# Kernel optimization log

Hardware: AMD Instinct MI355X
Metric: run time of the kernel (lower is better)

Reference implementation:

```python
import jax, jax.numpy as jnp
import numpy as np

BUCKET_SIZE = 64
LOOK_BACKWARD = 1
LOOK_FORWARD = 0  # causal => no look forward
CAUSAL = True


def look_around(x, backward, forward, pad_value):
    # x: [b, buckets, bucket_size, ...]; pads along the bucket axis and concats
    # shifted windows along the intra-bucket axis (dim=2), matching torch look_around.
    t = x.shape[1]
    pad_cfg = ((0, 0), (backward, forward)) + ((0, 0),) * (x.ndim - 2)
    padded = jnp.pad(x, pad_cfg, constant_values=pad_value)
    return jnp.concatenate([padded[:, i:i + t] for i in range(forward + backward + 1)], axis=2)


def setup_inputs() -> dict:
    key = jax.random.key(0)
    kq, kk, kv = jax.random.split(key, 3)
    shape = (4, 16, 4096, 64)  # [batch, heads, seq, head_dim]
    q = jax.random.normal(kq, shape, dtype=jnp.float32)
    k = jax.random.normal(kk, shape, dtype=jnp.float32)
    v = jax.random.normal(kv, shape, dtype=jnp.float32)
    return {"q": q, "k": k, "v": v}


def reference(q, k, v):
    shape = q.shape
    # merge batch and heads
    merge = lambda t: t.reshape(-1, t.shape[-2], t.shape[-1])
    q, k, v = merge(q), merge(k), merge(v)
    b, t, e = q.shape
    assert t % BUCKET_SIZE == 0
    buckets = t // BUCKET_SIZE

    ticker = jnp.arange(t, dtype=jnp.int32)[None, :]          # [1, t]
    b_t = ticker.reshape(1, buckets, BUCKET_SIZE)              # [1, buckets, bucket]

    bucket_fn = lambda x: x.reshape(b, buckets, BUCKET_SIZE, e)
    bq, bk, bv = bucket_fn(q), bucket_fn(k), bucket_fn(v)

    bk = look_around(bk, LOOK_BACKWARD, LOOK_FORWARD, 0.0)
    bv = look_around(bv, LOOK_BACKWARD, LOOK_FORWARD, 0.0)
    bq_t = b_t                                                 # query positions
    bq_k = look_around(b_t, LOOK_BACKWARD, LOOK_FORWARD, -1)   # key positions, -1 = pad

    scale = e ** (-0.5)
    dots = jnp.einsum('bnie,bnje->bnij', bq, bk) * scale
    mask_value = -jnp.finfo(dots.dtype).max

    if CAUSAL:
        causal_mask = bq_t[:, :, :, None] < bq_k[:, :, None, :]
        dots = jnp.where(causal_mask, mask_value, dots)

    pad_mask = bq_k[:, :, None, :] == -1
    dots = jnp.where(pad_mask, mask_value, dots)

    attn = jax.nn.softmax(dots, axis=-1)
    out = jnp.einsum('bnij,bnje->bnie', attn, bv)
    return out.reshape(shape)
```

## Files before the change

kernel.cpp:

```cpp
#include <hip/hip_runtime.h>
#include <hip/hip_bf16.h>

typedef __attribute__((ext_vector_type(8))) __bf16 bf16x8;
typedef __attribute__((ext_vector_type(4))) float f32x4;

#define SEQ   4096
#define HDIM  64
#define BKT   64

__device__ __forceinline__ unsigned f2bf_u(float f) {
    unsigned u = __float_as_uint(f);
    u += 0x7FFFu + ((u >> 16) & 1u);
    return u >> 16;
}
__device__ __forceinline__ unsigned pk2(float a, float b) {
    return f2bf_u(a) | (f2bf_u(b) << 16);
}
__device__ __forceinline__ int swzV(int row) {
    return ((row & 7) ^ ((row >> 3) & 7)) << 4;
}

__global__ void __launch_bounds__(256, 4) local_attn_kernel(
    const float* __restrict__ q, const float* __restrict__ k,
    const float* __restrict__ v, float* __restrict__ out)
{
    __shared__ __align__(16) unsigned short sK[128 * 64];
    __shared__ __align__(16) unsigned short sVt[64 * 128];

    const int tid = threadIdx.x;
    const int bid0 = blockIdx.x;
    const int lg = (bid0 & 7) * 512 + (bid0 >> 3);
    const int bh = lg >> 6;
    const int bucket = lg & 63;

    const int qoff = (bh * SEQ + bucket * BKT) * HDIM;
    const int koff = qoff - BKT * HDIM;
    const int fix0 = (bucket == 0) ? (BKT * HDIM) : 0;

    const int lane = tid & 63;
    const int wid  = tid >> 6;
    const int g = lane >> 4, m = lane & 15;
    const int g4 = g * 4;
    const int qbase = wid * 16;

    char* const sKb = reinterpret_cast<char*>(sK);
    char* const sVb = reinterpret_cast<char*>(sVt);

    f32x4 kreg[8], vreg[8], qreg[4];
    #pragma unroll
    for (int i = 0; i < 8; ++i) {
        const float* p = k + koff + ((i < 4) ? fix0 : 0) + i * 1024 + tid * 4;
        asm volatile("global_load_dwordx4 %0, %1, off"
                     : "=v"(kreg[i]) : "v"(p) : "memory");
    }
    #pragma unroll
    for (int i = 0; i < 8; ++i) {
        const int kb = i * 16 + wid * 4;
        const float* p = v + koff + ((i < 4) ? fix0 : 0) + (kb + g) * HDIM + m * 4;
        asm volatile("global_load_dwordx4 %0, %1, off"
                     : "=v"(vreg[i]) : "v"(p) : "memory");
    }
    #pragma unroll
    for (int h = 0; h < 2; ++h) {
        const float* qp = q + qoff + (qbase + m) * HDIM + h * 32 + g * 8;
        asm volatile("global_load_dwordx4 %0, %1, off"
                     : "=v"(qreg[2 * h]) : "v"(qp) : "memory");
        asm volatile("global_load_dwordx4 %0, %1, off"
                     : "=v"(qreg[2 * h + 1]) : "v"(qp + 4) : "memory");
    }

    asm volatile("s_waitcnt vmcnt(12)" ::: "memory");
    __builtin_amdgcn_sched_barrier(0);
    #pragma unroll
    for (int i = 0; i < 8; ++i) {
        const int flat = i * 1024 + tid * 4;
        const int row = flat >> 6, col = flat & 63;
        uint2 p;
        p.x = pk2(kreg[i][0], kreg[i][1]);
        p.y = pk2(kreg[i][2], kreg[i][3]);
        const int byte = (row * 128 + col * 2) ^ ((row & 7) << 4);
        *reinterpret_cast<uint2*>(sKb + byte) = p;
    }

    asm volatile("s_waitcnt vmcnt(4)" ::: "memory");
    __builtin_amdgcn_sched_barrier(0);
    #pragma unroll
    for (int i = 0; i < 8; ++i) {
        const int kb = i * 16 + wid * 4;
        const f32x4 f = vreg[i];
        const unsigned P0 = pk2(f[0], f[1]);
        const unsigned P1 = pk2(f[2], f[3]);
        const unsigned own  = (g < 2) ? P0 : P1;
        const unsigned send = (g < 2) ? P1 : P0;
        const unsigned R = __shfl_xor(send, 32);
        const unsigned T = __shfl_xor(own, 16);
        const unsigned U = __shfl_xor(R, 16);
        const unsigned A0 = (g < 2) ? own : R;
        const unsigned A1 = (g < 2) ? T : U;
        const unsigned A2 = (g < 2) ? R : own;
        const unsigned A3 = (g < 2) ? U : T;
        const int sdx = g & 1;
        const unsigned k0 = sdx ? A1 : A0, k1 = sdx ? A0 : A1;
        const unsigned k2 = sdx ? A3 : A2, k3 = sdx ? A2 : A3;
        const unsigned G0 = sdx ? ((k0 >> 16) | (k1 & 0xFFFF0000u)) : ((k0 & 0xFFFFu) | (k1 << 16));
        const unsigned G1 = sdx ? ((k2 >> 16) | (k3 & 0xFFFF0000u)) : ((k2 & 0xFFFFu) | (k3 << 16));
        const int er = m * 4 + g;
        const int byte = (er * 256 + kb * 2) ^ swzV(er);
        uint2 p; p.x = G0; p.y = G1;
        *reinterpret_cast<uint2*>(sVb + byte) = p;
    }

    asm volatile("s_waitcnt vmcnt(0)" ::: "memory");
    __builtin_amdgcn_sched_barrier(0);
    const float scale = 0.125f * 1.44269504f;
    bf16x8 bq[2];
    #pragma unroll
    for (int h = 0; h < 2; ++h) {
        uint4 u;
        u.x = pk2(qreg[2 * h][0] * scale, qreg[2 * h][1] * scale);
        u.y = pk2(qreg[2 * h][2] * scale, qreg[2 * h][3] * scale);
        u.z = pk2(qreg[2 * h + 1][0] * scale, qreg[2 * h + 1][1] * scale);
        u.w = pk2(qreg[2 * h + 1][2] * scale, qreg[2 * h + 1][3] * scale);
        bq[h] = __builtin_bit_cast(bf16x8, u);
    }
    __syncthreads();

    f32x4 acc[8];
    #pragma unroll
    for (int c = 0; c < 8; ++c) acc[c] = (f32x4){0.f, 0.f, 0.f, 0.f};
    __builtin_amdgcn_s_setprio(1);
    #pragma unroll
    for (int c = 0; c < 8; ++c) {
        const int krow = c * 16 + m;
        #pragma unroll
        for (int h = 0; h < 2; ++h) {
            const int byte = (krow * 128 + h * 64 + g * 16) ^ ((m & 7) << 4);
            const bf16x8 ak = *reinterpret_cast<const bf16x8*>(sKb + byte);
            acc[c] = __builtin_amdgcn_mfma_f32_16x16x32_bf16(ak, bq[h], acc[c], 0, 0, 0);
        }
    }
    __builtin_amdgcn_s_setprio(0);

    const int qb = qbase + m;
    float mx = -3e38f;
    #pragma unroll
    for (int c = 0; c < 8; ++c) {
        #pragma unroll
        for (int r = 0; r < 4; ++r) {
            const int kk = c * 16 + g4 + r;
            const bool dead = (c >= 4) ? (kk - 64 > qb) : (bucket == 0);
            const float s = dead ? -1e30f : acc[c][r];
            acc[c][r] = s;
            mx = fmaxf(mx, s);
        }
    }
    mx = fmaxf(mx, __shfl_xor(mx, 16));
    mx = fmaxf(mx, __shfl_xor(mx, 32));
    float sum = 0.f;
    uint2 pb[8];
    #pragma unroll
    for (int c = 0; c < 8; ++c) {
        const float p0 = __builtin_amdgcn_exp2f(acc[c][0] - mx);
        const float p1 = __builtin_amdgcn_exp2f(acc[c][1] - mx);
        const float p2 = __builtin_amdgcn_exp2f(acc[c][2] - mx);
        const float p3 = __builtin_amdgcn_exp2f(acc[c][3] - mx);
        sum += (p0 + p1) + (p2 + p3);
        pb[c].x = pk2(p0, p1);
        pb[c].y = pk2(p2, p3);
    }
    sum += __shfl_xor(sum, 16);
    sum += __shfl_xor(sum, 32);
    const float rl = 1.0f / sum;

    const int l0 = m + ((g & 1) << 5);
    const int l1 = l0 + 16;
    const bool hi2 = (g >> 1) != 0;
    bf16x8 bp[4];
    #pragma unroll
    for (int kt = 0; kt < 4; ++kt) {
        const unsigned a0x = __shfl(pb[2 * kt].x, l0),     a0y = __shfl(pb[2 * kt].y, l0);
        const unsigned a1x = __shfl(pb[2 * kt + 1].x, l0), a1y = __shfl(pb[2 * kt + 1].y, l0);
        const unsigned b0x = __shfl(pb[2 * kt].x, l1),     b0y = __shfl(pb[2 * kt].y, l1);
        const unsigned b1x = __shfl(pb[2 * kt + 1].x, l1), b1y = __shfl(pb[2 * kt + 1].y, l1);
        uint4 u;
        u.x = hi2 ? a1x : a0x;
        u.y = hi2 ? a1y : a0y;
        u.z = hi2 ? b1x : b0x;
        u.w = hi2 ? b1y : b0y;
        bp[kt] = __builtin_bit_cast(bf16x8, u);
    }

    f32x4 oacc[4];
    #pragma unroll
    for (int et = 0; et < 4; ++et) oacc[et] = (f32x4){0.f, 0.f, 0.f, 0.f};
    __builtin_amdgcn_s_setprio(1);
    #pragma unroll
    for (int et = 0; et < 4; ++et) {
        const int row = et * 16 + m;
        #pragma unroll
        for (int kt = 0; kt < 4; ++kt) {
            const int byte = (row * 256 + kt * 64 + g * 16) ^ swzV(row);
            const bf16x8 av = *reinterpret_cast<const bf16x8*>(sVb + byte);
            oacc[et] = __builtin_amdgcn_mfma_f32_16x16x32_bf16(av, bp[kt], oacc[et], 0, 0, 0);
        }
    }
    __builtin_amdgcn_s_setprio(0);

    const int qrow = qbase + m;
    #pragma unroll
    for (int et = 0; et < 4; ++et) {
        f32x4 o = oacc[et];
        o[0] *= rl; o[1] *= rl; o[2] *= rl; o[3] *= rl;
        *reinterpret_cast<float4*>(out + qoff + qrow * HDIM + et * 16 + g4) =
            *reinterpret_cast<float4*>(&o);
    }
}

extern "C" void kernel_launch(void* const* d_in, const int* in_sizes, int n_in,
                              void* d_out, int out_size, void* d_ws, size_t ws_size,
                              hipStream_t stream) {
    const float* q = (const float*)d_in[0];
    const float* k = (const float*)d_in[1];
    const float* v = (const float*)d_in[2];
    float* out = (float*)d_out;
    const int bh = in_sizes[0] / (SEQ * HDIM);
    const int nblocks = bh * (SEQ / BKT);
    hipLaunchKernelGGL(local_attn_kernel, dim3(nblocks), dim3(256), 0, stream,
                       q, k, v, out);
}
```

Measured before the change: 46.04 us.

## Process strips of four buckets per block with double-buffered K/V reuse

```diff
diff --git a/kernel.cpp b/kernel.cpp
--- a/kernel.cpp
+++ b/kernel.cpp
@@ -7,6 +7,8 @@
 #define SEQ   4096
 #define HDIM  64
 #define BKT   64
+#define STRIP 4
+#define SLOTB 8192
 
 __device__ __forceinline__ unsigned f2bf_u(float f) {
     unsigned u = __float_as_uint(f);
@@ -20,199 +22,263 @@
     return ((row & 7) ^ ((row >> 3) & 7)) << 4;
 }
 
+__device__ __forceinline__ void vtrans_write(char* sVb, int slotbyte, int kl,
+                                             f32x4 f, int g, int m) {
+    const unsigned P0 = pk2(f[0], f[1]);
+    const unsigned P1 = pk2(f[2], f[3]);
+    const unsigned own  = (g < 2) ? P0 : P1;
+    const unsigned send = (g < 2) ? P1 : P0;
+    const unsigned R = __shfl_xor(send, 32);
+    const unsigned T = __shfl_xor(own, 16);
+    const unsigned U = __shfl_xor(R, 16);
+    const unsigned A0 = (g < 2) ? own : R;
+    const unsigned A1 = (g < 2) ? T : U;
+    const unsigned A2 = (g < 2) ? R : own;
+    const unsigned A3 = (g < 2) ? U : T;
+    const int sdx = g & 1;
+    const unsigned k0 = sdx ? A1 : A0, k1 = sdx ? A0 : A1;
+    const unsigned k2 = sdx ? A3 : A2, k3 = sdx ? A2 : A3;
+    const unsigned G0 = sdx ? ((k0 >> 16) | (k1 & 0xFFFF0000u)) : ((k0 & 0xFFFFu) | (k1 << 16));
+    const unsigned G1 = sdx ? ((k2 >> 16) | (k3 & 0xFFFF0000u)) : ((k2 & 0xFFFFu) | (k3 << 16));
+    const int er = m * 4 + g;
+    const int byte = slotbyte + ((er * 128 + kl * 2) ^ swzV(er));
+    uint2 p; p.x = G0; p.y = G1;
+    *reinterpret_cast<uint2*>(sVb + byte) = p;
+}
+
 __global__ void __launch_bounds__(256, 4) local_attn_kernel(
     const float* __restrict__ q, const float* __restrict__ k,
     const float* __restrict__ v, float* __restrict__ out)
 {
-    __shared__ __align__(16) unsigned short sK[128 * 64];
-    __shared__ __align__(16) unsigned short sVt[64 * 128];
+    __shared__ __align__(16) unsigned short sK[2 * 64 * 64];
+    __shared__ __align__(16) unsigned short sVt[2 * 64 * 64];
 
     const int tid = threadIdx.x;
-    const int bid0 = blockIdx.x;
-    const int lg = (bid0 & 7) * 512 + (bid0 >> 3);
-    const int bh = lg >> 6;
-    const int bucket = lg & 63;
-
-    const int qoff = (bh * SEQ + bucket * BKT) * HDIM;
-    const int koff = qoff - BKT * HDIM;
-    const int fix0 = (bucket == 0) ? (BKT * HDIM) : 0;
+    const int bid = blockIdx.x;
+    const int lg = (bid & 7) * 128 + (bid >> 3);
+    const int bh = lg >> 4;
+    const int strip = lg & 15;
+    const int b0 = strip * STRIP;
+    const int base = bh * SEQ * HDIM;
 
     const int lane = tid & 63;
     const int wid  = tid >> 6;
     const int g = lane >> 4, m = lane & 15;
     const int g4 = g * 4;
     const int qbase = wid * 16;
+    const int qb = qbase + m;
 
     char* const sKb = reinterpret_cast<char*>(sK);
     char* const sVb = reinterpret_cast<char*>(sVt);
 
-    f32x4 kreg[8], vreg[8], qreg[4];
-    #pragma unroll
-    for (int i = 0; i < 8; ++i) {
-        const float* p = k + koff + ((i < 4) ? fix0 : 0) + i * 1024 + tid * 4;
-        asm volatile("global_load_dwordx4 %0, %1, off"
-                     : "=v"(kreg[i]) : "v"(p) : "memory");
-    }
-    #pragma unroll
-    for (int i = 0; i < 8; ++i) {
-        const int kb = i * 16 + wid * 4;
-        const float* p = v + koff + ((i < 4) ? fix0 : 0) + (kb + g) * HDIM + m * 4;
-        asm volatile("global_load_dwordx4 %0, %1, off"
-                     : "=v"(vreg[i]) : "v"(p) : "memory");
-    }
-    #pragma unroll
-    for (int h = 0; h < 2; ++h) {
-        const float* qp = q + qoff + (qbase + m) * HDIM + h * 32 + g * 8;
-        asm volatile("global_load_dwordx4 %0, %1, off"
-                     : "=v"(qreg[2 * h]) : "v"(qp) : "memory");
-        asm volatile("global_load_dwordx4 %0, %1, off"
-                     : "=v"(qreg[2 * h + 1]) : "v"(qp + 4) : "memory");
-    }
-
-    asm volatile("s_waitcnt vmcnt(12)" ::: "memory");
-    __builtin_amdgcn_sched_barrier(0);
-    #pragma unroll
-    for (int i = 0; i < 8; ++i) {
-        const int flat = i * 1024 + tid * 4;
-        const int row = flat >> 6, col = flat & 63;
-        uint2 p;
-        p.x = pk2(kreg[i][0], kreg[i][1]);
-        p.y = pk2(kreg[i][2], kreg[i][3]);
-        const int byte = (row * 128 + col * 2) ^ ((row & 7) << 4);
-        *reinterpret_cast<uint2*>(sKb + byte) = p;
-    }
-
-    asm volatile("s_waitcnt vmcnt(4)" ::: "memory");
-    __builtin_amdgcn_sched_barrier(0);
-    #pragma unroll
-    for (int i = 0; i < 8; ++i) {
-        const int kb = i * 16 + wid * 4;
-        const f32x4 f = vreg[i];
-        const unsigned P0 = pk2(f[0], f[1]);
-        const unsigned P1 = pk2(f[2], f[3]);
-        const unsigned own  = (g < 2) ? P0 : P1;
-        const unsigned send = (g < 2) ? P1 : P0;
-        const unsigned R = __shfl_xor(send, 32);
-        const unsigned T = __shfl_xor(own, 16);
-        const unsigned U = __shfl_xor(R, 16);
-        const unsigned A0 = (g < 2) ? own : R;
-        const unsigned A1 = (g < 2) ? T : U;
-        const unsigned A2 = (g < 2) ? R : own;
-        const unsigned A3 = (g < 2) ? U : T;
-        const int sdx = g & 1;
-        const unsigned k0 = sdx ? A1 : A0, k1 = sdx ? A0 : A1;
-        const unsigned k2 = sdx ? A3 : A2, k3 = sdx ? A2 : A3;
-        const unsigned G0 = sdx ? ((k0 >> 16) | (k1 & 0xFFFF0000u)) : ((k0 & 0xFFFFu) | (k1 << 16));
-        const unsigned G1 = sdx ? ((k2 >> 16) | (k3 & 0xFFFF0000u)) : ((k2 & 0xFFFFu) | (k3 << 16));
-        const int er = m * 4 + g;
-        const int byte = (er * 256 + kb * 2) ^ swzV(er);
-        uint2 p; p.x = G0; p.y = G1;
-        *reinterpret_cast<uint2*>(sVb + byte) = p;
-    }
-
-    asm volatile("s_waitcnt vmcnt(0)" ::: "memory");
-    __builtin_amdgcn_sched_barrier(0);
     const float scale = 0.125f * 1.44269504f;
     bf16x8 bq[2];
+
+    {
+        const int fix0 = (strip == 0) ? (BKT * HDIM) : 0;
+        const int win0 = base + (b0 - 1) * BKT * HDIM;
+        f32x4 kreg[8], vreg[8], qreg[4];
+        #pragma unroll
+        for (int i = 0; i < 8; ++i) {
+            const float* p = k + win0 + ((i < 4) ? fix0 : 0) + i * 1024 + tid * 4;
+            asm volatile("global_load_dwordx4 %0, %1, off" : "=v"(kreg[i]) : "v"(p) : "memory");
+        }
+        #pragma unroll
+        for (int i = 0; i < 8; ++i) {
+            const int kb = i * 16 + wid * 4;
+            const float* p = v + win0 + ((i < 4) ? fix0 : 0) + (kb + g) * HDIM + m * 4;
+            asm volatile("global_load_dwordx4 %0, %1, off" : "=v"(vreg[i]) : "v"(p) : "memory");
+        }
+        const int qoff0 = base + b0 * BKT * HDIM;
+        #pragma unroll
+        for (int h = 0; h < 2; ++h) {
+            const float* qp = q + qoff0 + qb * HDIM + h * 32 + g * 8;
+            asm volatile("global_load_dwordx4 %0, %1, off" : "=v"(qreg[2 * h]) : "v"(qp) : "memory");
+            asm volatile("global_load_dwordx4 %0, %1, off" : "=v"(qreg[2 * h + 1]) : "v"(qp + 4) : "memory");
+        }
+        asm volatile("s_waitcnt vmcnt(12)" ::: "memory");
+        __builtin_amdgcn_sched_barrier(0);
+        #pragma unroll
+        for (int i = 0; i < 8; ++i) {
+            const int flat = i * 1024 + tid * 4;
+            const int lr = (flat >> 6) & 63, col = flat & 63;
+            uint2 p;
+            p.x = pk2(kreg[i][0], kreg[i][1]);
+            p.y = pk2(kreg[i][2], kreg[i][3]);
+            const int byte = ((i < 4) ? SLOTB : 0) + ((lr * 128 + col * 2) ^ ((lr & 7) << 4));
+            *reinterpret_cast<uint2*>(sKb + byte) = p;
+        }
+        asm volatile("s_waitcnt vmcnt(4)" ::: "memory");
+        __builtin_amdgcn_sched_barrier(0);
+        #pragma unroll
+        for (int i = 0; i < 8; ++i) {
+            const int kl = (i * 16 + wid * 4) & 63;
+            vtrans_write(sVb, (i < 4) ? SLOTB : 0, kl, vreg[i], g, m);
+        }
+        asm volatile("s_waitcnt vmcnt(0)" ::: "memory");
+        __builtin_amdgcn_sched_barrier(0);
+        #pragma unroll
+        for (int h = 0; h < 2; ++h) {
+            uint4 u;
+            u.x = pk2(qreg[2 * h][0] * scale, qreg[2 * h][1] * scale);
+            u.y = pk2(qreg[2 * h][2] * scale, qreg[2 * h][3] * scale);
+            u.z = pk2(qreg[2 * h + 1][0] * scale, qreg[2 * h + 1][1] * scale);
+            u.w = pk2(qreg[2 * h + 1][2] * scale, qreg[2 * h + 1][3] * scale);
+            bq[h] = __builtin_bit_cast(bf16x8, u);
+        }
+        __syncthreads();
+    }
+
     #pragma unroll
-    for (int h = 0; h < 2; ++h) {
-        uint4 u;
-        u.x = pk2(qreg[2 * h][0] * scale, qreg[2 * h][1] * scale);
-        u.y = pk2(qreg[2 * h][2] * scale, qreg[2 * h][3] * scale);
-        u.z = pk2(qreg[2 * h + 1][0] * scale, qreg[2 * h + 1][1] * scale);
-        u.w = pk2(qreg[2 * h + 1][2] * scale, qreg[2 * h + 1][3] * scale);
-        bq[h] = __builtin_bit_cast(bf16x8, u);
-    }
-    __syncthreads();
-
-    f32x4 acc[8];
-    #pragma unroll
-    for (int c = 0; c < 8; ++c) acc[c] = (f32x4){0.f, 0.f, 0.f, 0.f};
-    __builtin_amdgcn_s_setprio(1);
-    #pragma unroll
-    for (int c = 0; c < 8; ++c) {
-        const int krow = c * 16 + m;
-        #pragma unroll
-        for (int h = 0; h < 2; ++h) {
-            const int byte = (krow * 128 + h * 64 + g * 16) ^ ((m & 7) << 4);
-            const bf16x8 ak = *reinterpret_cast<const bf16x8*>(sKb + byte);
-            acc[c] = __builtin_amdgcn_mfma_f32_16x16x32_bf16(ak, bq[h], acc[c], 0, 0, 0);
-        }
-    }
-    __builtin_amdgcn_s_setprio(0);
-
-    const int qb = qbase + m;
-    float mx = -3e38f;
-    #pragma unroll
-    for (int c = 0; c < 8; ++c) {
-        #pragma unroll
-        for (int r = 0; r < 4; ++r) {
-            const int kk = c * 16 + g4 + r;
-            const bool dead = (c >= 4) ? (kk - 64 > qb) : (bucket == 0);
-            const float s = dead ? -1e30f : acc[c][r];
-            acc[c][r] = s;
-            mx = fmaxf(mx, s);
-        }
-    }
-    mx = fmaxf(mx, __shfl_xor(mx, 16));
-    mx = fmaxf(mx, __shfl_xor(mx, 32));
-    float sum = 0.f;
-    uint2 pb[8];
-    #pragma unroll
-    for (int c = 0; c < 8; ++c) {
-        const float p0 = __builtin_amdgcn_exp2f(acc[c][0] - mx);
-        const float p1 = __builtin_amdgcn_exp2f(acc[c][1] - mx);
-        const float p2 = __builtin_amdgcn_exp2f(acc[c][2] - mx);
-        const float p3 = __builtin_amdgcn_exp2f(acc[c][3] - mx);
-        sum += (p0 + p1) + (p2 + p3);
-        pb[c].x = pk2(p0, p1);
-        pb[c].y = pk2(p2, p3);
-    }
-    sum += __shfl_xor(sum, 16);
-    sum += __shfl_xor(sum, 32);
-    const float rl = 1.0f / sum;
-
-    const int l0 = m + ((g & 1) << 5);
-    const int l1 = l0 + 16;
-    const bool hi2 = (g >> 1) != 0;
-    bf16x8 bp[4];
-    #pragma unroll
-    for (int kt = 0; kt < 4; ++kt) {
-        const unsigned a0x = __shfl(pb[2 * kt].x, l0),     a0y = __shfl(pb[2 * kt].y, l0);
-        const unsigned a1x = __shfl(pb[2 * kt + 1].x, l0), a1y = __shfl(pb[2 * kt + 1].y, l0);
-        const unsigned b0x = __shfl(pb[2 * kt].x, l1),     b0y = __shfl(pb[2 * kt].y, l1);
-        const unsigned b1x = __shfl(pb[2 * kt + 1].x, l1), b1y = __shfl(pb[2 * kt + 1].y, l1);
-        uint4 u;
-        u.x = hi2 ? a1x : a0x;
-        u.y = hi2 ? a1y : a0y;
-        u.z = hi2 ? b1x : b0x;
-        u.w = hi2 ? b1y : b0y;
-        bp[kt] = __builtin_bit_cast(bf16x8, u);
-    }
-
-    f32x4 oacc[4];
-    #pragma unroll
-    for (int et = 0; et < 4; ++et) oacc[et] = (f32x4){0.f, 0.f, 0.f, 0.f};
-    __builtin_amdgcn_s_setprio(1);
-    #pragma unroll
-    for (int et = 0; et < 4; ++et) {
-        const int row = et * 16 + m;
+    for (int j = 0; j < STRIP; ++j) {
+        const int qoffj = base + (b0 + j) * BKT * HDIM;
+        const int spre = ((j & 1) ^ 1) * SLOTB;
+        const int scur = (j & 1) * SLOTB;
+
+        f32x4 kn[4], vn[4], qn[4];
+        if (j < STRIP - 1) {
+            const int noff = qoffj + BKT * HDIM;
+            #pragma unroll
+            for (int i = 0; i < 4; ++i) {
+                const float* p = k + noff + i * 1024 + tid * 4;
+                asm volatile("global_load_dwordx4 %0, %1, off" : "=v"(kn[i]) : "v"(p) : "memory");
+            }
+            #pragma unroll
+            for (int i = 0; i < 4; ++i) {
+                const int kbl = i * 16 + wid * 4;
+                const float* p = v + noff + (kbl + g) * HDIM + m * 4;
+                asm volatile("global_load_dwordx4 %0, %1, off" : "=v"(vn[i]) : "v"(p) : "memory");
+            }
+            #pragma unroll
+            for (int h = 0; h < 2; ++h) {
+                const float* qp = q + noff + qb * HDIM + h * 32 + g * 8;
+                asm volatile("global_load_dwordx4 %0, %1, off" : "=v"(qn[2 * h]) : "v"(qp) : "memory");
+                asm volatile("global_load_dwordx4 %0, %1, off" : "=v"(qn[2 * h + 1]) : "v"(qp + 4) : "memory");
+            }
+        }
+
+        f32x4 acc[8];
+        #pragma unroll
+        for (int c = 0; c < 8; ++c) acc[c] = (f32x4){0.f, 0.f, 0.f, 0.f};
+        __builtin_amdgcn_s_setprio(1);
+        #pragma unroll
+        for (int c = 0; c < 8; ++c) {
+            const int lr = (c & 3) * 16 + m;
+            const int sb = (c < 4) ? spre : scur;
+            #pragma unroll
+            for (int h = 0; h < 2; ++h) {
+                const int byte = sb + ((lr * 128 + h * 64 + g * 16) ^ ((m & 7) << 4));
+                const bf16x8 ak = *reinterpret_cast<const bf16x8*>(sKb + byte);
+                acc[c] = __builtin_amdgcn_mfma_f32_16x16x32_bf16(ak, bq[h], acc[c], 0, 0, 0);
+            }
+        }
+        __builtin_amdgcn_s_setprio(0);
+
+        const bool dead_prev = (strip == 0 && j == 0);
+        float mx = -3e38f;
+        #pragma unroll
+        for (int c = 0; c < 8; ++c) {
+            #pragma unroll
+            for (int r = 0; r < 4; ++r) {
+                const int kk = c * 16 + g4 + r;
+                const bool dead = (c >= 4) ? (kk - 64 > qb) : dead_prev;
+                const float s = dead ? -1e30f : acc[c][r];
+                acc[c][r] = s;
+                mx = fmaxf(mx, s);
+            }
+        }
+        mx = fmaxf(mx, __shfl_xor(mx, 16));
+        mx = fmaxf(mx, __shfl_xor(mx, 32));
+        float sum = 0.f;
+        uint2 pb[8];
+        #pragma unroll
+        for (int c = 0; c < 8; ++c) {
+            const float p0 = __builtin_amdgcn_exp2f(acc[c][0] - mx);
+            const float p1 = __builtin_amdgcn_exp2f(acc[c][1] - mx);
+            const float p2 = __builtin_amdgcn_exp2f(acc[c][2] - mx);
+            const float p3 = __builtin_amdgcn_exp2f(acc[c][3] - mx);
+            sum += (p0 + p1) + (p2 + p3);
+            pb[c].x = pk2(p0, p1);
+            pb[c].y = pk2(p2, p3);
+        }
+        sum += __shfl_xor(sum, 16);
+        sum += __shfl_xor(sum, 32);
+        const float rl = 1.0f / sum;
+
+        const int l0 = m + ((g & 1) << 5);
+        const int l1 = l0 + 16;
+        const bool hi2 = (g >> 1) != 0;
+        bf16x8 bp[4];
         #pragma unroll
         for (int kt = 0; kt < 4; ++kt) {
-            const int byte = (row * 256 + kt * 64 + g * 16) ^ swzV(row);
-            const bf16x8 av = *reinterpret_cast<const bf16x8*>(sVb + byte);
-            oacc[et] = __builtin_amdgcn_mfma_f32_16x16x32_bf16(av, bp[kt], oacc[et], 0, 0, 0);
-        }
-    }
-    __builtin_amdgcn_s_setprio(0);
-
-    const int qrow = qbase + m;
-    #pragma unroll
-    for (int et = 0; et < 4; ++et) {
-        f32x4 o = oacc[et];
-        o[0] *= rl; o[1] *= rl; o[2] *= rl; o[3] *= rl;
-        *reinterpret_cast<float4*>(out + qoff + qrow * HDIM + et * 16 + g4) =
-            *reinterpret_cast<float4*>(&o);
+            const unsigned a0x = __shfl(pb[2 * kt].x, l0),     a0y = __shfl(pb[2 * kt].y, l0);
+            const unsigned a1x = __shfl(pb[2 * kt + 1].x, l0), a1y = __shfl(pb[2 * kt + 1].y, l0);
+            const unsigned b0x = __shfl(pb[2 * kt].x, l1),     b0y = __shfl(pb[2 * kt].y, l1);
+            const unsigned b1x = __shfl(pb[2 * kt + 1].x, l1), b1y = __shfl(pb[2 * kt + 1].y, l1);
+            uint4 u;
+            u.x = hi2 ? a1x : a0x;
+            u.y = hi2 ? a1y : a0y;
+            u.z = hi2 ? b1x : b0x;
+            u.w = hi2 ? b1y : b0y;
+            bp[kt] = __builtin_bit_cast(bf16x8, u);
+        }
+
+        f32x4 oacc[4];
+        #pragma unroll
+        for (int et = 0; et < 4; ++et) oacc[et] = (f32x4){0.f, 0.f, 0.f, 0.f};
+        __builtin_amdgcn_s_setprio(1);
+        #pragma unroll
+        for (int et = 0; et < 4; ++et) {
+            const int row = et * 16 + m;
+            #pragma unroll
+            for (int kt = 0; kt < 4; ++kt) {
+                const int sb = (kt < 2) ? spre : scur;
+                const int kl = (kt & 1) * 32 + g * 8;
+                const int byte = sb + ((row * 128 + kl * 2) ^ swzV(row));
+                const bf16x8 av = *reinterpret_cast<const bf16x8*>(sVb + byte);
+                oacc[et] = __builtin_amdgcn_mfma_f32_16x16x32_bf16(av, bp[kt], oacc[et], 0, 0, 0);
+            }
+        }
+        __builtin_amdgcn_s_setprio(0);
+
+        #pragma unroll
+        for (int et = 0; et < 4; ++et) {
+            f32x4 o = oacc[et];
+            o[0] *= rl; o[1] *= rl; o[2] *= rl; o[3] *= rl;
+            *reinterpret_cast<float4*>(out + qoffj + qb * HDIM + et * 16 + g4) =
+                *reinterpret_cast<float4*>(&o);
+        }
+
+        if (j < STRIP - 1) {
+            __syncthreads();
+            asm volatile("s_waitcnt vmcnt(4)" ::: "memory");
+            __builtin_amdgcn_sched_barrier(0);
+            #pragma unroll
+            for (int i = 0; i < 4; ++i) {
+                const int flat = i * 1024 + tid * 4;
+                const int lr = flat >> 6, col = flat & 63;
+                uint2 p;
+                p.x = pk2(kn[i][0], kn[i][1]);
+                p.y = pk2(kn[i][2], kn[i][3]);
+                const int byte = spre + ((lr * 128 + col * 2) ^ ((lr & 7) << 4));
+                *reinterpret_cast<uint2*>(sKb + byte) = p;
+            }
+            #pragma unroll
+            for (int i = 0; i < 4; ++i) {
+                const int kbl = i * 16 + wid * 4;
+                vtrans_write(sVb, spre, kbl, vn[i], g, m);
+            }
+            #pragma unroll
+            for (int h = 0; h < 2; ++h) {
+                uint4 u;
+                u.x = pk2(qn[2 * h][0] * scale, qn[2 * h][1] * scale);
+                u.y = pk2(qn[2 * h][2] * scale, qn[2 * h][3] * scale);
+                u.z = pk2(qn[2 * h + 1][0] * scale, qn[2 * h + 1][1] * scale);
+                u.w = pk2(qn[2 * h + 1][2] * scale, qn[2 * h + 1][3] * scale);
+                bq[h] = __builtin_bit_cast(bf16x8, u);
+            }
+            __syncthreads();
+        }
     }
 }
 
@@ -224,7 +290,7 @@
     const float* v = (const float*)d_in[2];
     float* out = (float*)d_out;
     const int bh = in_sizes[0] / (SEQ * HDIM);
-    const int nblocks = bh * (SEQ / BKT);
+    const int nblocks = bh * (SEQ / BKT / STRIP);
     hipLaunchKernelGGL(local_attn_kernel, dim3(nblocks), dim3(256), 0, stream,
                        q, k, v, out);
 }
```

After: 59.61 us. +29.5%, slower.
